# Kernel tuning notes

Hardware: AMD Instinct MI355X
Metric: run time of the kernel (lower is better)

The kernel has to match this reference:

```python
import jax, jax.numpy as jnp
import numpy as np

B, MENU, N, M = 4096, 256, 8, 16


def setup_inputs() -> dict:
    key = jax.random.key(0)
    k1, k2, k3, k4 = jax.random.split(key, 4)
    input_bids = jax.random.uniform(k1, (B, N, M), dtype=jnp.float32)
    allocs = jax.random.uniform(k2, (B, MENU, N, M), dtype=jnp.float32)
    # bidder weights must be strictly positive (divided by in payments)
    w = jax.random.uniform(k3, (B, N), dtype=jnp.float32, minval=0.5, maxval=1.5)
    b = jax.random.normal(k4, (B, MENU), dtype=jnp.float32)
    softmax_temp = jnp.asarray(100.0, dtype=jnp.float32)
    return {"input_bids": input_bids, "allocs": allocs, "w": w, "b": b,
            "softmax_temp": softmax_temp}


def reference(input_bids, allocs, w, b, softmax_temp):
    Bsz, n, m = input_bids.shape
    # append the "null" menu entry (zero allocation, zero boost)
    allocs = jnp.concatenate([allocs, jnp.zeros((Bsz, 1, n, m), allocs.dtype)], axis=1)  # B,S,n,m
    b = jnp.concatenate([b, jnp.zeros((Bsz, 1), b.dtype)], axis=1)                        # B,S

    # utility of each agent under each menu entry
    util = jnp.einsum('bsnm,bnm->bsn', allocs, input_bids)        # B,S,n
    per_agent_welfare = w[:, None, :] * util                      # B,S,n
    total_welfare = per_agent_welfare.sum(-1)                     # B,S

    alloc_choice = jax.nn.softmax((total_welfare + b) * softmax_temp, axis=-1)  # B,S
    item_allocation = jnp.einsum('bs,bsnm->bnm', alloc_choice, allocs)          # B,n,m
    chosen_welfare = jnp.einsum('bsn,bs->bn', per_agent_welfare, alloc_choice)  # B,n

    # leave-one-out (VCG-style) payments, vectorized over the removed agent i
    mask = 1.0 - jnp.eye(n, dtype=per_agent_welfare.dtype)        # n,n; row i zeros agent i
    removed_welfare = per_agent_welfare[None] * mask[:, None, None, :]  # i,B,S,n
    total_removed = removed_welfare.sum(-1)                       # i,B,S
    removed_choice = jax.nn.softmax((total_removed + b[None]) * softmax_temp, axis=-1)  # i,B,S

    removed_chosen_sum = jnp.einsum('ibsn,ibs->ib', removed_welfare, removed_choice)  # i,B
    masked_chosen_sum = jnp.einsum('bn,in->ib', chosen_welfare, mask)                 # i,B
    removed_b = jnp.einsum('ibs,bs->ib', removed_choice, b)                           # i,B
    alloc_b = jnp.einsum('bs,bs->b', alloc_choice, b)                                 # B

    payments = (removed_chosen_sum + removed_b - masked_chosen_sum - alloc_b[None]) / w.T  # n,B
    return alloc_choice, item_allocation, payments, allocs
```

## Files before the change

kernel.cpp:

```cpp
#include <hip/hip_runtime.h>

#define NAGENTS 8
#define NM 128
#define MENU 256
#define SFULL 257

typedef float f32x4 __attribute__((ext_vector_type(4)));

#define BAR() asm volatile("s_waitcnt lgkmcnt(0)\n\ts_barrier" ::: "memory")

__device__ __forceinline__ float wredmax(float v) {
#pragma unroll
    for (int o = 32; o; o >>= 1) v = fmaxf(v, __shfl_xor(v, o));
    return v;
}
__device__ __forceinline__ float wredsum(float v) {
#pragma unroll
    for (int o = 32; o; o >>= 1) v += __shfl_xor(v, o);
    return v;
}

__global__ __launch_bounds__(256, 8) void cama_kernel(
    const float* __restrict__ bids,
    const float* __restrict__ allocs,
    const float* __restrict__ wvec,
    const float* __restrict__ bvec,
    const float* __restrict__ tempp,
    float* __restrict__ out, int Bsz)
{
    __shared__ float lds_pwT[NAGENTS * MENU];
    __shared__ float lds_tot[MENU];
    __shared__ float lds_bb[MENU];
    __shared__ float lds_bbt[MENU];
    __shared__ float lds_ch[SFULL];
    __shared__ __align__(16) float4 lds_accs[4][32];
    __shared__ __align__(8)  float2 lds_mz[4][32];
    __shared__ float lds_rcs[NAGENTS], lds_rb[NAGENTS], lds_cw[NAGENTS];
    __shared__ float lds_ab;

    const int u = threadIdx.x;
    const int lane = u & 63;
    const int wave = u >> 6;
    const int c = u & 31;
    const int n = c >> 2;
    const int su = u >> 5;
    const size_t bb_ = (size_t)blockIdx.x;

    float* out_choice = out;
    float* out_item   = out + (size_t)Bsz * SFULL;
    float* out_pay    = out_item + (size_t)Bsz * NM;
    float* out_all    = out_pay + (size_t)NAGENTS * Bsz;
    f32x4* out_all4   = (f32x4*)out_all + bb_ * 8224;
    const f32x4* src4 = (const f32x4*)allocs + bb_ * 8192;

    const float temp = tempp[0];
    {
        float bv = bvec[bb_ * MENU + u];
        lds_bb[u]  = bv;
        lds_bbt[u] = bv * temp;
    }
    const float4 q4 = ((const float4*)(bids + bb_ * NM))[c];
    const float w_n = wvec[bb_ * NAGENTS + n];
    BAR();

    float m_r = -1e30f, Z_r = 0.f;
    float4 acc = make_float4(0.f, 0.f, 0.f, 0.f);
#pragma unroll 4
    for (int k = 0; k < 32; ++k) {
        const int idx = (k << 8) + u;
        f32x4 a4 = src4[idx];
        out_all4[idx] = a4;
        const int s = (k << 3) + su;
        float util = a4[0]*q4.x + a4[1]*q4.y + a4[2]*q4.z + a4[3]*q4.w;
        util += __shfl_xor(util, 1);
        util += __shfl_xor(util, 2);
        float pwv = w_n * util;
        if ((u & 3) == 0) lds_pwT[(n << 8) + (s ^ (n << 2))] = pwv;
        float t = pwv;
        t += __shfl_xor(t, 4);
        t += __shfl_xor(t, 8);
        t += __shfl_xor(t, 16);
        if (c == 0) lds_tot[s] = t;
        float x = fmaf(t, temp, lds_bbt[s]);
        if (x > m_r + 8.f) {
            float sc = __expf(m_r - x);
            Z_r *= sc;
            acc.x *= sc; acc.y *= sc; acc.z *= sc; acc.w *= sc;
            m_r = x;
        }
        float p = __expf(x - m_r);
        Z_r += p;
        acc.x = fmaf(p, a4[0], acc.x);
        acc.y = fmaf(p, a4[1], acc.y);
        acc.z = fmaf(p, a4[2], acc.z);
        acc.w = fmaf(p, a4[3], acc.w);
    }
    if (u < 32) {
        f32x4 z4 = {0.f, 0.f, 0.f, 0.f};
        out_all4[8192 + u] = z4;
    }

    {
        float mo = __shfl_xor(m_r, 32);
        float Zo = __shfl_xor(Z_r, 32);
        float ax = __shfl_xor(acc.x, 32), ay = __shfl_xor(acc.y, 32);
        float az = __shfl_xor(acc.z, 32), aw = __shfl_xor(acc.w, 32);
        float mn = fmaxf(m_r, mo);
        float s0 = __expf(m_r - mn), s1 = __expf(mo - mn);
        Z_r = Z_r * s0 + Zo * s1;
        acc.x = acc.x * s0 + ax * s1;
        acc.y = acc.y * s0 + ay * s1;
        acc.z = acc.z * s0 + az * s1;
        acc.w = acc.w * s0 + aw * s1;
        if (lane < 32) {
            lds_accs[wave][c] = acc;
            lds_mz[wave][c] = make_float2(mn, Z_r);
        }
    }
    BAR();

    for (int t = wave; t < 9; t += 4) {
        if (t == 0) {
            float xs[4], bl[4], es[4];
            float mx = -1e30f;
#pragma unroll
            for (int c4 = 0; c4 < 4; ++c4) {
                int v = (c4 << 6) | lane;
                bl[c4] = lds_bb[v];
                float x = (lds_tot[v] + bl[c4]) * temp;
                xs[c4] = x; mx = fmaxf(mx, x);
            }
            mx = fmaxf(wredmax(mx), 0.f);
            float se = 0.f, sab = 0.f;
#pragma unroll
            for (int c4 = 0; c4 < 4; ++c4) {
                es[c4] = __expf(xs[c4] - mx);
                se += es[c4]; sab += es[c4] * bl[c4];
            }
            float en = __expf(-mx);
            se = wredsum(se) + en;
            sab = wredsum(sab);
            float inv = 1.f / se;
#pragma unroll
            for (int c4 = 0; c4 < 4; ++c4) {
                int v = (c4 << 6) | lane;
                float chv = es[c4] * inv;
                lds_ch[v] = chv;
                out_choice[bb_ * SFULL + v] = chv;
            }
            if (lane == 0) {
                float chn = en * inv;
                lds_ch[MENU] = chn;
                out_choice[bb_ * SFULL + MENU] = chn;
                lds_ab = sab * inv;
            }
        } else {
            const int i = t - 1;
            float xs[4], trs[4], bl[4];
            float mx = -1e30f;
#pragma unroll
            for (int c4 = 0; c4 < 4; ++c4) {
                int v = (c4 << 6) | lane;
                bl[c4] = lds_bb[v];
                float tr = lds_tot[v] - lds_pwT[(i << 8) + (v ^ (i << 2))];
                trs[c4] = tr;
                float x = (tr + bl[c4]) * temp;
                xs[c4] = x; mx = fmaxf(mx, x);
            }
            mx = fmaxf(wredmax(mx), 0.f);
            float se = 0.f, s1 = 0.f, s2 = 0.f;
#pragma unroll
            for (int c4 = 0; c4 < 4; ++c4) {
                float e = __expf(xs[c4] - mx);
                se += e; s1 += e * trs[c4]; s2 += e * bl[c4];
            }
            se = wredsum(se) + __expf(-mx);
            s1 = wredsum(s1);
            s2 = wredsum(s2);
            if (lane == 0) { lds_rcs[i] = s1 / se; lds_rb[i] = s2 / se; }
        }
    }
    BAR();

    for (int i = wave; i < NAGENTS; i += 4) {
        float cwv = 0.f;
#pragma unroll
        for (int c4 = 0; c4 < 4; ++c4) {
            int v = (c4 << 6) | lane;
            cwv += lds_ch[v] * lds_pwT[(i << 8) + (v ^ (i << 2))];
        }
        cwv = wredsum(cwv);
        if (lane == 0) lds_cw[i] = cwv;
    }
    if (u < 32) {
        float4 A = lds_accs[0][u];
        float2 mz = lds_mz[0][u];
        float M = mz.x, Z = mz.y;
#pragma unroll
        for (int j = 1; j < 4; ++j) {
            float4 Aj = lds_accs[j][u];
            float2 mzj = lds_mz[j][u];
            float mn = fmaxf(M, mzj.x);
            float s0 = __expf(M - mn), s1 = __expf(mzj.x - mn);
            Z = Z * s0 + mzj.y * s1;
            A.x = A.x * s0 + Aj.x * s1;
            A.y = A.y * s0 + Aj.y * s1;
            A.z = A.z * s0 + Aj.z * s1;
            A.w = A.w * s0 + Aj.w * s1;
            M = mn;
        }
        float mn = fmaxf(M, 0.f);
        float s0 = __expf(M - mn);
        Z = Z * s0 + __expf(-mn);
        float inv = 1.f / Z;
        s0 *= inv;
        ((float4*)(out_item + bb_ * NM))[u] =
            make_float4(A.x * s0, A.y * s0, A.z * s0, A.w * s0);
    }
    BAR();

    if (u < NAGENTS) {
        float ctot = 0.f;
#pragma unroll
        for (int k = 0; k < NAGENTS; ++k) ctot += lds_cw[k];
        float pay = (lds_rcs[u] + lds_rb[u] - (ctot - lds_cw[u]) - lds_ab)
                    / wvec[bb_ * NAGENTS + u];
        out_pay[(size_t)u * Bsz + bb_] = pay;
    }
}

extern "C" void kernel_launch(void* const* d_in, const int* in_sizes, int n_in,
                              void* d_out, int out_size, void* d_ws, size_t ws_size,
                              hipStream_t stream) {
    const float* bids   = (const float*)d_in[0];
    const float* allocs = (const float*)d_in[1];
    const float* wvec   = (const float*)d_in[2];
    const float* bvec   = (const float*)d_in[3];
    const float* tempp  = (const float*)d_in[4];
    float* out = (float*)d_out;
    const int Bsz = in_sizes[0] / NM;
    cama_kernel<<<Bsz, 256, 0, stream>>>(bids, allocs, wvec, bvec, tempp,
                                         out, Bsz);
}
```

Measured before the change: 236.8 us.

## Fuse leave-one-out and chosen-welfare softmaxes into the streaming online-softmax loop

Moves the leave-one-out softmax statistics, the alloc_b and chosen-welfare sums into the main streaming loop as extra per-thread online-softmax accumulators, then merges them across half-waves and waves. This removes the per-agent pwT LDS table, the post-loop wave reductions and one barrier phase. The cost is more exp and FMA work per loop iteration, since the rescale now runs unconditionally for two softmaxes, in a loop that is largely memory-bound.

```diff
diff --git a/kernel.cpp b/kernel.cpp
--- a/kernel.cpp
+++ b/kernel.cpp
@@ -8,17 +8,6 @@
 typedef float f32x4 __attribute__((ext_vector_type(4)));
 
 #define BAR() asm volatile("s_waitcnt lgkmcnt(0)\n\ts_barrier" ::: "memory")
-
-__device__ __forceinline__ float wredmax(float v) {
-#pragma unroll
-    for (int o = 32; o; o >>= 1) v = fmaxf(v, __shfl_xor(v, o));
-    return v;
-}
-__device__ __forceinline__ float wredsum(float v) {
-#pragma unroll
-    for (int o = 32; o; o >>= 1) v += __shfl_xor(v, o);
-    return v;
-}
 
 __global__ __launch_bounds__(256, 8) void cama_kernel(
     const float* __restrict__ bids,
@@ -28,21 +17,22 @@
     const float* __restrict__ tempp,
     float* __restrict__ out, int Bsz)
 {
-    __shared__ float lds_pwT[NAGENTS * MENU];
     __shared__ float lds_tot[MENU];
     __shared__ float lds_bb[MENU];
-    __shared__ float lds_bbt[MENU];
-    __shared__ float lds_ch[SFULL];
     __shared__ __align__(16) float4 lds_accs[4][32];
-    __shared__ __align__(8)  float2 lds_mz[4][32];
+    __shared__ __align__(16) float4 lds_w1[4];
+    __shared__ __align__(16) float4 lds_loo[4][8];
+    __shared__ float lds_scw[4][8];
     __shared__ float lds_rcs[NAGENTS], lds_rb[NAGENTS], lds_cw[NAGENTS];
     __shared__ float lds_ab;
+    __shared__ float2 lds_mzf;
 
     const int u = threadIdx.x;
     const int lane = u & 63;
     const int wave = u >> 6;
     const int c = u & 31;
     const int n = c >> 2;
+    const int mq = u & 3;
     const int su = u >> 5;
     const size_t bb_ = (size_t)blockIdx.x;
 
@@ -54,46 +44,52 @@
     const f32x4* src4 = (const f32x4*)allocs + bb_ * 8192;
 
     const float temp = tempp[0];
-    {
-        float bv = bvec[bb_ * MENU + u];
-        lds_bb[u]  = bv;
-        lds_bbt[u] = bv * temp;
-    }
+    lds_bb[u] = bvec[bb_ * MENU + u];
     const float4 q4 = ((const float4*)(bids + bb_ * NM))[c];
     const float w_n = wvec[bb_ * NAGENTS + n];
     BAR();
 
-    float m_r = -1e30f, Z_r = 0.f;
-    float4 acc = make_float4(0.f, 0.f, 0.f, 0.f);
+    float M1 = -1e30f, Z1 = 0.f, Sab = 0.f, Scw = 0.f;
+    float4 A = make_float4(0.f, 0.f, 0.f, 0.f);
+    float M2 = -1e30f, Z2 = 0.f, S1 = 0.f, S2 = 0.f;
+
 #pragma unroll 4
     for (int k = 0; k < 32; ++k) {
         const int idx = (k << 8) + u;
         f32x4 a4 = src4[idx];
         out_all4[idx] = a4;
         const int s = (k << 3) + su;
+        const float bbs = lds_bb[s];
         float util = a4[0]*q4.x + a4[1]*q4.y + a4[2]*q4.z + a4[3]*q4.w;
         util += __shfl_xor(util, 1);
         util += __shfl_xor(util, 2);
         float pwv = w_n * util;
-        if ((u & 3) == 0) lds_pwT[(n << 8) + (s ^ (n << 2))] = pwv;
         float t = pwv;
         t += __shfl_xor(t, 4);
         t += __shfl_xor(t, 8);
         t += __shfl_xor(t, 16);
         if (c == 0) lds_tot[s] = t;
-        float x = fmaf(t, temp, lds_bbt[s]);
-        if (x > m_r + 8.f) {
-            float sc = __expf(m_r - x);
-            Z_r *= sc;
-            acc.x *= sc; acc.y *= sc; acc.z *= sc; acc.w *= sc;
-            m_r = x;
-        }
-        float p = __expf(x - m_r);
-        Z_r += p;
-        acc.x = fmaf(p, a4[0], acc.x);
-        acc.y = fmaf(p, a4[1], acc.y);
-        acc.z = fmaf(p, a4[2], acc.z);
-        acc.w = fmaf(p, a4[3], acc.w);
+        float x = (t + bbs) * temp;
+        float mn = fmaxf(M1, x);
+        float sc = __expf(M1 - mn);
+        float p  = __expf(x - mn);
+        Z1  = Z1*sc + p;
+        A.x = A.x*sc + p*a4[0];
+        A.y = A.y*sc + p*a4[1];
+        A.z = A.z*sc + p*a4[2];
+        A.w = A.w*sc + p*a4[3];
+        Sab = Sab*sc + p*bbs;
+        Scw = Scw*sc + p*pwv;
+        M1 = mn;
+        float tr = t - pwv;
+        float x2 = (tr + bbs) * temp;
+        float mn2 = fmaxf(M2, x2);
+        float sc2 = __expf(M2 - mn2);
+        float p2  = __expf(x2 - mn2);
+        Z2 = Z2*sc2 + p2;
+        S1 = S1*sc2 + p2*tr;
+        S2 = S2*sc2 + p2*bbs;
+        M2 = mn2;
     }
     if (u < 32) {
         f32x4 z4 = {0.f, 0.f, 0.f, 0.f};
@@ -101,124 +97,113 @@
     }
 
     {
-        float mo = __shfl_xor(m_r, 32);
-        float Zo = __shfl_xor(Z_r, 32);
-        float ax = __shfl_xor(acc.x, 32), ay = __shfl_xor(acc.y, 32);
-        float az = __shfl_xor(acc.z, 32), aw = __shfl_xor(acc.w, 32);
-        float mn = fmaxf(m_r, mo);
-        float s0 = __expf(m_r - mn), s1 = __expf(mo - mn);
-        Z_r = Z_r * s0 + Zo * s1;
-        acc.x = acc.x * s0 + ax * s1;
-        acc.y = acc.y * s0 + ay * s1;
-        acc.z = acc.z * s0 + az * s1;
-        acc.w = acc.w * s0 + aw * s1;
+        float Mo = __shfl_xor(M1, 32), Zo = __shfl_xor(Z1, 32);
+        float Sabo = __shfl_xor(Sab, 32), Scwo = __shfl_xor(Scw, 32);
+        float ax = __shfl_xor(A.x, 32), ay = __shfl_xor(A.y, 32);
+        float az = __shfl_xor(A.z, 32), aw = __shfl_xor(A.w, 32);
+        float mn = fmaxf(M1, Mo);
+        float s0 = __expf(M1 - mn), s1 = __expf(Mo - mn);
+        Z1  = Z1*s0  + Zo*s1;
+        Sab = Sab*s0 + Sabo*s1;
+        Scw = Scw*s0 + Scwo*s1;
+        A.x = A.x*s0 + ax*s1;  A.y = A.y*s0 + ay*s1;
+        A.z = A.z*s0 + az*s1;  A.w = A.w*s0 + aw*s1;
+        M1 = mn;
+
+        float Mo2 = __shfl_xor(M2, 32), Zo2 = __shfl_xor(Z2, 32);
+        float S1o = __shfl_xor(S1, 32), S2o = __shfl_xor(S2, 32);
+        float mn2 = fmaxf(M2, Mo2);
+        float t0 = __expf(M2 - mn2), t1 = __expf(Mo2 - mn2);
+        Z2 = Z2*t0 + Zo2*t1;
+        S1 = S1*t0 + S1o*t1;
+        S2 = S2*t0 + S2o*t1;
+        M2 = mn2;
+
         if (lane < 32) {
-            lds_accs[wave][c] = acc;
-            lds_mz[wave][c] = make_float2(mn, Z_r);
+            lds_accs[wave][c] = make_float4(A.x, A.y, A.z, A.w);
+            if (c == 0) lds_w1[wave] = make_float4(M1, Z1, Sab, 0.f);
+            if (mq == 0) {
+                lds_scw[wave][n] = Scw;
+                lds_loo[wave][n] = make_float4(M2, Z2, S1, S2);
+            }
         }
     }
     BAR();
 
-    for (int t = wave; t < 9; t += 4) {
-        if (t == 0) {
-            float xs[4], bl[4], es[4];
-            float mx = -1e30f;
-#pragma unroll
-            for (int c4 = 0; c4 < 4; ++c4) {
-                int v = (c4 << 6) | lane;
-                bl[c4] = lds_bb[v];
-                float x = (lds_tot[v] + bl[c4]) * temp;
-                xs[c4] = x; mx = fmaxf(mx, x);
-            }
-            mx = fmaxf(wredmax(mx), 0.f);
-            float se = 0.f, sab = 0.f;
-#pragma unroll
-            for (int c4 = 0; c4 < 4; ++c4) {
-                es[c4] = __expf(xs[c4] - mx);
-                se += es[c4]; sab += es[c4] * bl[c4];
-            }
-            float en = __expf(-mx);
-            se = wredsum(se) + en;
-            sab = wredsum(sab);
-            float inv = 1.f / se;
-#pragma unroll
-            for (int c4 = 0; c4 < 4; ++c4) {
-                int v = (c4 << 6) | lane;
-                float chv = es[c4] * inv;
-                lds_ch[v] = chv;
-                out_choice[bb_ * SFULL + v] = chv;
-            }
-            if (lane == 0) {
-                float chn = en * inv;
-                lds_ch[MENU] = chn;
-                out_choice[bb_ * SFULL + MENU] = chn;
-                lds_ab = sab * inv;
-            }
-        } else {
-            const int i = t - 1;
-            float xs[4], trs[4], bl[4];
-            float mx = -1e30f;
-#pragma unroll
-            for (int c4 = 0; c4 < 4; ++c4) {
-                int v = (c4 << 6) | lane;
-                bl[c4] = lds_bb[v];
-                float tr = lds_tot[v] - lds_pwT[(i << 8) + (v ^ (i << 2))];
-                trs[c4] = tr;
-                float x = (tr + bl[c4]) * temp;
-                xs[c4] = x; mx = fmaxf(mx, x);
-            }
-            mx = fmaxf(wredmax(mx), 0.f);
-            float se = 0.f, s1 = 0.f, s2 = 0.f;
-#pragma unroll
-            for (int c4 = 0; c4 < 4; ++c4) {
-                float e = __expf(xs[c4] - mx);
-                se += e; s1 += e * trs[c4]; s2 += e * bl[c4];
-            }
-            se = wredsum(se) + __expf(-mx);
-            s1 = wredsum(s1);
-            s2 = wredsum(s2);
-            if (lane == 0) { lds_rcs[i] = s1 / se; lds_rb[i] = s2 / se; }
-        }
+    if (u < 32) {
+        float4 w1 = lds_w1[0];
+        float Mm = w1.x, Zm = w1.y, Sabm = w1.z;
+        float4 Am = lds_accs[0][u];
+#pragma unroll
+        for (int j = 1; j < 4; ++j) {
+            float4 wj = lds_w1[j];
+            float4 Aj = lds_accs[j][u];
+            float mn = fmaxf(Mm, wj.x);
+            float s0 = __expf(Mm - mn), s1 = __expf(wj.x - mn);
+            Zm   = Zm*s0   + wj.y*s1;
+            Sabm = Sabm*s0 + wj.z*s1;
+            Am.x = Am.x*s0 + Aj.x*s1;  Am.y = Am.y*s0 + Aj.y*s1;
+            Am.z = Am.z*s0 + Aj.z*s1;  Am.w = Am.w*s0 + Aj.w*s1;
+            Mm = mn;
+        }
+        float M1f = fmaxf(Mm, 0.f);
+        float s0 = __expf(Mm - M1f);
+        float Z1f = Zm*s0 + __expf(-M1f);
+        float inv = 1.f / Z1f;
+        float sf = s0 * inv;
+        ((float4*)(out_item + bb_ * NM))[u] =
+            make_float4(Am.x*sf, Am.y*sf, Am.z*sf, Am.w*sf);
+        if (u == 0) {
+            lds_ab = Sabm * sf;
+            lds_mzf = make_float2(M1f, inv);
+        }
+    } else if (u < 40) {
+        const int i = u - 32;
+        float4 L = lds_loo[0][i];
+        float Mm = L.x, Zm = L.y, S1m = L.z, S2m = L.w;
+#pragma unroll
+        for (int j = 1; j < 4; ++j) {
+            float4 Lj = lds_loo[j][i];
+            float mn = fmaxf(Mm, Lj.x);
+            float s0 = __expf(Mm - mn), s1 = __expf(Lj.x - mn);
+            Zm  = Zm*s0  + Lj.y*s1;
+            S1m = S1m*s0 + Lj.z*s1;
+            S2m = S2m*s0 + Lj.w*s1;
+            Mm = mn;
+        }
+        float M2f = fmaxf(Mm, 0.f);
+        float s0 = __expf(Mm - M2f);
+        float Z2f = Zm*s0 + __expf(-M2f);
+        lds_rcs[i] = S1m*s0 / Z2f;
+        lds_rb[i]  = S2m*s0 / Z2f;
+    } else if (u < 48) {
+        const int i = u - 40;
+        float4 w1 = lds_w1[0];
+        float Mm = w1.x, Zm = w1.y;
+        float Sm = lds_scw[0][i];
+#pragma unroll
+        for (int j = 1; j < 4; ++j) {
+            float4 wj = lds_w1[j];
+            float mn = fmaxf(Mm, wj.x);
+            float s0 = __expf(Mm - mn), s1 = __expf(wj.x - mn);
+            Zm = Zm*s0 + wj.y*s1;
+            Sm = Sm*s0 + lds_scw[j][i]*s1;
+            Mm = mn;
+        }
+        float M1f = fmaxf(Mm, 0.f);
+        float s0 = __expf(Mm - M1f);
+        float Z1f = Zm*s0 + __expf(-M1f);
+        lds_cw[i] = Sm*s0 / Z1f;
     }
     BAR();
 
-    for (int i = wave; i < NAGENTS; i += 4) {
-        float cwv = 0.f;
-#pragma unroll
-        for (int c4 = 0; c4 < 4; ++c4) {
-            int v = (c4 << 6) | lane;
-            cwv += lds_ch[v] * lds_pwT[(i << 8) + (v ^ (i << 2))];
-        }
-        cwv = wredsum(cwv);
-        if (lane == 0) lds_cw[i] = cwv;
-    }
-    if (u < 32) {
-        float4 A = lds_accs[0][u];
-        float2 mz = lds_mz[0][u];
-        float M = mz.x, Z = mz.y;
-#pragma unroll
-        for (int j = 1; j < 4; ++j) {
-            float4 Aj = lds_accs[j][u];
-            float2 mzj = lds_mz[j][u];
-            float mn = fmaxf(M, mzj.x);
-            float s0 = __expf(M - mn), s1 = __expf(mzj.x - mn);
-            Z = Z * s0 + mzj.y * s1;
-            A.x = A.x * s0 + Aj.x * s1;
-            A.y = A.y * s0 + Aj.y * s1;
-            A.z = A.z * s0 + Aj.z * s1;
-            A.w = A.w * s0 + Aj.w * s1;
-            M = mn;
-        }
-        float mn = fmaxf(M, 0.f);
-        float s0 = __expf(M - mn);
-        Z = Z * s0 + __expf(-mn);
-        float inv = 1.f / Z;
-        s0 *= inv;
-        ((float4*)(out_item + bb_ * NM))[u] =
-            make_float4(A.x * s0, A.y * s0, A.z * s0, A.w * s0);
-    }
-    BAR();
-
+    {
+        float2 mzf = lds_mzf;
+        float x = (lds_tot[u] + lds_bb[u]) * temp;
+        out_choice[bb_ * SFULL + u] = __expf(x - mzf.x) * mzf.y;
+        if (u == 0)
+            out_choice[bb_ * SFULL + MENU] = __expf(-mzf.x) * mzf.y;
+    }
     if (u < NAGENTS) {
         float ctot = 0.f;
 #pragma unroll
```

Result: no change. 233.7 us (-1.3%).
